# Kernel optimization log

Measured on AMD Instinct MI355X. Metric: run time of the kernel, lower is better.

## Reference

```python
import jax, jax.numpy as jnp
import numpy as np

RADIUS = 5
EPS = 1e-08


def _box_blur(x, r):
    """Normalized (2r+1)x(2r+1) box filter with reflect padding, NCHW."""
    k = 2 * r + 1
    B, C, H, W = x.shape
    xp = jnp.pad(x, ((0, 0), (0, 0), (r, r), (r, r)), mode='reflect')
    y = xp.reshape(B * C, 1, H + 2 * r, W + 2 * r)
    kh = jnp.ones((1, 1, k, 1), x.dtype) / k
    kw = jnp.ones((1, 1, 1, k), x.dtype) / k
    y = jax.lax.conv_general_dilated(y, kh, (1, 1), 'VALID')
    y = jax.lax.conv_general_dilated(y, kw, (1, 1), 'VALID')
    return y.reshape(B, C, H, W)


def setup_inputs() -> dict:
    key = jax.random.key(0)
    k1, k2 = jax.random.split(key)
    feat = jax.random.uniform(k1, (8, 16, 512, 512), dtype=jnp.float32)
    img = jax.random.uniform(k2, (8, 1, 512, 512), dtype=jnp.float32)
    return {"feat": feat, "img": img}


def reference(feat, img):
    r, eps = RADIUS, EPS
    # scalar-guidance guided filter (guidance img has 1 channel)
    mean_I = _box_blur(img, r)                  # [B,1,H,W]
    mean_p = _box_blur(feat, r)                 # [B,D,H,W]
    corr_I = _box_blur(img * img, r)            # [B,1,H,W]
    corr_Ip = _box_blur(img * feat, r)          # [B,D,H,W]
    var_I = corr_I - mean_I * mean_I
    cov_Ip = corr_Ip - mean_I * mean_p
    a = cov_Ip / (var_I + eps)                  # [B,D,H,W]
    b = mean_p - a * mean_I                     # [B,D,H,W]
    mean_a = _box_blur(a, r)
    mean_b = _box_blur(b, r)
    return mean_a * img + mean_b
```

## Files before the change

### kernel.cpp

```cpp
#include <hip/hip_runtime.h>

#define HH 512
#define WW 512
#define HW (512*512)
#define NB 8
#define ND 16
#define TW 64
#define TH 64
#define VR 74
#define PT 86
#define GAP 20

__device__ __forceinline__ int reflect(int v) {
    if (v < 0) v = -v;
    if (v >= HH) v = 2*HH - 2 - v;
    return v;
}

__global__ __launch_bounds__(256) void img_stats(const float* __restrict__ img,
                                                 float2* __restrict__ miv) {
    const int VRs = 42, PTs = 86, THs = 32, TWs = 64;
    __shared__ __align__(16) float hBuf[2*VRs*PTs + 20];
    float* hF = hBuf;
    float* hP = hBuf + VRs*PTs + 20;

    int blk  = blockIdx.x;
    int tile = blk & 127;
    int b    = blk >> 7;
    int ty0  = (tile >> 3) * THs;
    int tx0  = (tile & 7)  * TWs;

    const float inv121 = 1.0f/121.0f;
    const float* ib = img + (size_t)b*HW;
    const int t = threadIdx.x;

    if (t < 252) {
        int seg = t / 84, col = t - seg*84;
        int gx = reflect(tx0 - 10 + col);
        const float* icol = ib + gx;
        int vr0 = seg*14;
        float rv[11], rq[11];
        float sv = 0.f, sq = 0.f;
        #pragma unroll
        for (int j = 0; j < 10; ++j) {
            int gy = reflect(ty0 - 10 + vr0 + j);
            float v = icol[gy*WW], q = v*v;
            rv[j] = v; rq[j] = q; sv += v; sq += q;
        }
        #pragma unroll
        for (int k = 0; k < 14; ++k) {
            int vr = vr0 + k;
            int gy = reflect(ty0 + vr);
            float v = icol[gy*WW], q = v*v;
            sv += v; sq += q;
            hF[vr*PTs + col] = sv;
            hP[vr*PTs + col] = sq;
            sv -= rv[k%11]; sq -= rq[k%11];
            rv[(k+10)%11] = v; rq[(k+10)%11] = q;
        }
    }
    __syncthreads();

    if (t < 168) {
        int arr = t & 1;
        int j2  = t >> 1;
        int seg = (j2 >= 42) ? 1 : 0;
        int vr  = j2 - seg*42;
        int xb = seg ? 38 : 0;
        int nout = seg ? 18 : 19;
        float* rA = (arr ? hP : hF) + vr*PTs;
        float2 ring[5];
        float T = 0.f;
        #pragma unroll
        for (int j = 0; j < 5; ++j) {
            float2 v = *(float2*)(rA + xb + 2*j);
            ring[j] = v; T += v.x + v.y;
        }
        #pragma unroll
        for (int k2 = 0; k2 < 19; ++k2) {
            if (k2 < nout) {
                int hc = xb + 2*k2;
                float2 p = *(float2*)(rA + hc + 10);
                float2 q = ring[k2 % 5];
                float O0 = T + p.x;
                float O1 = O0 + p.y - q.x;
                T = O1 - q.y;
                ring[k2 % 5] = p;
                float2 o; o.x = O0*inv121; o.y = O1*inv121;
                *(float2*)(rA + hc + 10*seg) = o;
            }
        }
    }
    __syncthreads();

    float2* mb = miv + (size_t)b*HW;
    for (int i = t; i < THs*TWs; i += 256) {
        int y = i >> 6, x = i & 63;
        int vr = y + 5, hc = x + 5;
        int slot = hc + ((hc >= 38) ? 10 : 0);
        float mI  = hF[vr*PTs + slot];
        float mII = hP[vr*PTs + slot];
        float var = mII - mI*mI;
        float2 o; o.x = mI; o.y = 1.0f / (var + 1e-8f);
        mb[(ty0 + y)*WW + tx0 + x] = o;
    }
}

__global__ __launch_bounds__(512) void guided_main(const float* __restrict__ feat,
                                                   const float* __restrict__ img,
                                                   const float2* __restrict__ miv,
                                                   float* __restrict__ out) {
    __shared__ __align__(16) float hBuf[2*VR*PT + GAP];
    float* hF = hBuf;
    float* hP = hBuf + VR*PT + GAP;

    int blk  = blockIdx.x;
    int tile = blk & 63;
    int bd   = blk >> 6;
    int b    = bd >> 4;
    int ty0  = (tile >> 3) * TH;
    int tx0  = (tile & 7)  * TW;

    const float inv121 = 1.0f/121.0f;
    const float* fb   = feat + (size_t)bd*HW;
    const float* ib   = img  + (size_t)b*HW;
    const float2* mivb = miv + (size_t)b*HW;
    const int t = threadIdx.x;

    if (t < 504) {
        int seg = t / 84, col = t - seg*84;
        int gx = reflect(tx0 - 10 + col);
        const float* fcol = fb + gx;
        const float* icol = ib + gx;
        int vr0 = seg*13;
        float rf[11], rp[11];
        float sf = 0.f, sp = 0.f;
        #pragma unroll
        for (int j = 0; j < 10; ++j) {
            int gy = reflect(ty0 - 10 + vr0 + j);
            float f = fcol[gy*WW], im = icol[gy*WW];
            float p = f*im;
            rf[j] = f; rp[j] = p; sf += f; sp += p;
        }
        #pragma unroll
        for (int k = 0; k < 13; ++k) {
            int vr = vr0 + k;
            if (vr < VR) {
                int gy = reflect(ty0 + vr);
                float f = fcol[gy*WW], im = icol[gy*WW];
                float p = f*im;
                sf += f; sp += p;
                hF[vr*PT + col] = sf;
                hP[vr*PT + col] = sp;
                sf -= rf[k%11]; sp -= rp[k%11];
                rf[(k+10)%11] = f; rp[(k+10)%11] = p;
            }
        }
    }
    __syncthreads();

    if (t < 296) {
        int arr = t & 1;
        int j2  = t >> 1;
        int seg = (j2 >= 74) ? 1 : 0;
        int vr  = j2 - seg*74;
        int xb = seg ? 38 : 0;
        int nout = seg ? 18 : 19;
        float* rA = (arr ? hP : hF) + vr*PT;
        float2 ring[5];
        float T = 0.f;
        #pragma unroll
        for (int j = 0; j < 5; ++j) {
            float2 v = *(float2*)(rA + xb + 2*j);
            ring[j] = v; T += v.x + v.y;
        }
        #pragma unroll
        for (int k2 = 0; k2 < 19; ++k2) {
            if (k2 < nout) {
                int hc = xb + 2*k2;
                float2 p = *(float2*)(rA + hc + 10);
                float2 q = ring[k2 % 5];
                float O0 = T + p.x;
                float O1 = O0 + p.y - q.x;
                T = O1 - q.y;
                ring[k2 % 5] = p;
                float2 o; o.x = O0*inv121; o.y = O1*inv121;
                *(float2*)(rA + hc + 10*seg) = o;
            }
        }
    }
    __syncthreads();

    for (int i = t; i < VR*37; i += 512) {
        int y = i / 37, c2 = i - y*37;
        int x0 = 2*c2;
        int slot = x0 + ((x0 >= 38) ? 10 : 0);
        float* pF = &hF[y*PT + slot];
        float* pP = &hP[y*PT + slot];
        float2 mp2  = *(float2*)pF;
        float2 cip2 = *(float2*)pP;
        int gy = reflect(ty0 - 5 + y);
        const float2* mrow = mivb + gy*WW;
        int gx0 = tx0 - 5 + x0;
        float2 g0 = mrow[reflect(gx0)];
        float2 g1 = mrow[reflect(gx0+1)];
        float a0 = (cip2.x - g0.x*mp2.x) * g0.y;
        float b0 = mp2.x - a0*g0.x;
        float a1 = (cip2.y - g1.x*mp2.y) * g1.y;
        float b1 = mp2.y - a1*g1.x;
        float2 oa; oa.x = a0; oa.y = a1;
        float2 ob2; ob2.x = b0; ob2.y = b1;
        *(float2*)pF = oa;
        *(float2*)pP = ob2;
    }
    __syncthreads();

    if (t < 148) {
        int arr = t & 1;
        int j2  = t >> 1;
        int seg = (j2 >= 37) ? 1 : 0;
        int c2  = j2 - seg*37;
        int x0 = 2*c2;
        int slotc = x0 + ((x0 >= 38) ? 10 : 0);
        int y0 = seg*32;
        float* A = (arr ? hP : hF);
        float2 ring[11];
        float sx = 0.f, sy = 0.f;
        #pragma unroll
        for (int j = 0; j < 10; ++j) {
            float2 v = *(float2*)(A + (y0+j)*PT + slotc);
            ring[j] = v; sx += v.x; sy += v.y;
        }
        #pragma unroll
        for (int k = 0; k < 32; ++k) {
            int y = y0 + k;
            float2 v = *(float2*)(A + (y+10)*PT + slotc);
            sx += v.x; sy += v.y;
            int wrow = y + 10*seg;
            float2 o; o.x = sx; o.y = sy;
            *(float2*)(A + wrow*PT + slotc) = o;
            sx -= ring[k%11].x; sy -= ring[k%11].y;
            ring[(k+10)%11] = v;
        }
    }
    __syncthreads();

    if (t < 256) {
        int arr = t & 1;
        int r2  = t >> 1;
        int seg = r2 >> 6, row = r2 & 63;
        int prow = row + ((row >= 32) ? 10 : 0);
        float* rA = (arr ? hP : hF) + prow*PT;
        int xb = seg*32;
        float2 ring[5];
        float T = 0.f;
        #pragma unroll
        for (int j = 0; j < 5; ++j) {
            int idx = xb + 2*j;
            int sl = idx + ((idx >= 38) ? 10 : 0);
            float2 v = *(float2*)(rA + sl);
            ring[j] = v; T += v.x + v.y;
        }
        #pragma unroll
        for (int k2 = 0; k2 < 16; ++k2) {
            int x = xb + 2*k2;
            int idx = x + 10;
            int sl = idx + ((idx >= 38) ? 10 : 0);
            float2 p = *(float2*)(rA + sl);
            float2 q = ring[k2 % 5];
            float O0 = T + p.x;
            float O1 = O0 + p.y - q.x;
            T = O1 - q.y;
            ring[k2 % 5] = p;
            int wcol = x + 20*seg;
            float2 o; o.x = O0; o.y = O1;
            *(float2*)(rA + wcol) = o;
        }
    }
    __syncthreads();

    float* ob = out + (size_t)bd*HW;
    for (int i = t; i < TH*32; i += 512) {
        int y = i >> 5, c2 = i & 31;
        int x0 = 2*c2;
        int prow = y + ((y >= 32) ? 10 : 0);
        int wcol = (x0 < 32) ? x0 : x0 + 20;
        float2 ma2 = *(float2*)(&hF[prow*PT + wcol]);
        float2 mb2 = *(float2*)(&hP[prow*PT + wcol]);
        int gy = ty0 + y;
        float2 im2 = *(const float2*)(ib + gy*WW + tx0 + x0);
        float2 o;
        o.x = (ma2.x*im2.x + mb2.x)*inv121;
        o.y = (ma2.y*im2.y + mb2.y)*inv121;
        *(float2*)(ob + gy*WW + tx0 + x0) = o;
    }
}

extern "C" void kernel_launch(void* const* d_in, const int* in_sizes, int n_in,
                              void* d_out, int out_size, void* d_ws, size_t ws_size,
                              hipStream_t stream) {
    const float* feat = (const float*)d_in[0];
    const float* img  = (const float*)d_in[1];
    float* out  = (float*)d_out;
    float2* miv = (float2*)d_ws;

    img_stats<<<NB*128, 256, 0, stream>>>(img, miv);
    guided_main<<<NB*ND*64, 512, 0, stream>>>(feat, img, miv, out);
}
```

Baseline: 149.3 us.

## Interleave F/P planes in shared memory as float2 pairs for wider LDS access

Replaces the two separate shared-memory planes (box sums of feat and feat*img) with a single interleaved buffer in which each column holds an (F,P) pair. The horizontal passes now process both arrays in one thread using float4 loads and stores, which halves the threads used in those phases. The a/b computation and the final output read a single float4 instead of two float2 loads. This cuts LDS instruction count but changes the bank-access patterns, and the horizontal passes now run with half as many active threads.

```diff
diff --git a/kernel.cpp b/kernel.cpp
--- a/kernel.cpp
+++ b/kernel.cpp
@@ -8,8 +8,7 @@
 #define TW 64
 #define TH 64
 #define VR 74
-#define PT 86
-#define GAP 20
+#define PTW 172
 
 __device__ __forceinline__ int reflect(int v) {
     if (v < 0) v = -v;
@@ -110,9 +109,7 @@
                                                    const float* __restrict__ img,
                                                    const float2* __restrict__ miv,
                                                    float* __restrict__ out) {
-    __shared__ __align__(16) float hBuf[2*VR*PT + GAP];
-    float* hF = hBuf;
-    float* hP = hBuf + VR*PT + GAP;
+    __shared__ __align__(16) float S[VR*PTW];
 
     int blk  = blockIdx.x;
     int tile = blk & 63;
@@ -150,8 +147,8 @@
                 float f = fcol[gy*WW], im = icol[gy*WW];
                 float p = f*im;
                 sf += f; sp += p;
-                hF[vr*PT + col] = sf;
-                hP[vr*PT + col] = sp;
+                float2 st; st.x = sf; st.y = sp;
+                *(float2*)(S + vr*PTW + 2*col) = st;
                 sf -= rf[k%11]; sp -= rp[k%11];
                 rf[(k+10)%11] = f; rp[(k+10)%11] = p;
             }
@@ -159,139 +156,128 @@
     }
     __syncthreads();
 
-    if (t < 296) {
-        int arr = t & 1;
-        int j2  = t >> 1;
-        int seg = (j2 >= 74) ? 1 : 0;
-        int vr  = j2 - seg*74;
-        int xb = seg ? 38 : 0;
+    if (t < 148) {
+        int seg = (t >= 74) ? 1 : 0;
+        int vr  = t - seg*74;
+        float* row = S + vr*PTW;
+        int xbu = seg*19;
         int nout = seg ? 18 : 19;
-        float* rA = (arr ? hP : hF) + vr*PT;
-        float2 ring[5];
-        float T = 0.f;
+        float4 ring[5];
+        float TF = 0.f, TP = 0.f;
         #pragma unroll
         for (int j = 0; j < 5; ++j) {
-            float2 v = *(float2*)(rA + xb + 2*j);
-            ring[j] = v; T += v.x + v.y;
-        }
-        #pragma unroll
-        for (int k2 = 0; k2 < 19; ++k2) {
-            if (k2 < nout) {
-                int hc = xb + 2*k2;
-                float2 p = *(float2*)(rA + hc + 10);
-                float2 q = ring[k2 % 5];
-                float O0 = T + p.x;
-                float O1 = O0 + p.y - q.x;
-                T = O1 - q.y;
-                ring[k2 % 5] = p;
-                float2 o; o.x = O0*inv121; o.y = O1*inv121;
-                *(float2*)(rA + hc + 10*seg) = o;
+            float4 v = *(float4*)(row + 4*(xbu + j));
+            ring[j] = v; TF += v.x + v.z; TP += v.y + v.w;
+        }
+        #pragma unroll
+        for (int k = 0; k < 19; ++k) {
+            if (k < nout) {
+                float4 p = *(float4*)(row + 4*(xbu + 5 + k));
+                float4 q = ring[k % 5];
+                float O0f = TF + p.x;
+                float O1f = O0f + p.z - q.x;
+                TF = O1f - q.z;
+                float O0p = TP + p.y;
+                float O1p = O0p + p.w - q.y;
+                TP = O1p - q.w;
+                ring[k % 5] = p;
+                float4 o;
+                o.x = O0f*inv121; o.y = O0p*inv121;
+                o.z = O1f*inv121; o.w = O1p*inv121;
+                *(float4*)(row + 4*(k + xbu + 5*seg)) = o;
             }
         }
     }
     __syncthreads();
 
     for (int i = t; i < VR*37; i += 512) {
-        int y = i / 37, c2 = i - y*37;
-        int x0 = 2*c2;
-        int slot = x0 + ((x0 >= 38) ? 10 : 0);
-        float* pF = &hF[y*PT + slot];
-        float* pP = &hP[y*PT + slot];
-        float2 mp2  = *(float2*)pF;
-        float2 cip2 = *(float2*)pP;
+        int y = i / 37, u = i - y*37;
+        int su = u + ((u >= 19) ? 5 : 0);
+        float* cell = S + y*PTW + 4*su;
+        float4 mc = *(float4*)cell;
         int gy = reflect(ty0 - 5 + y);
         const float2* mrow = mivb + gy*WW;
-        int gx0 = tx0 - 5 + x0;
+        int gx0 = tx0 - 5 + 2*u;
         float2 g0 = mrow[reflect(gx0)];
         float2 g1 = mrow[reflect(gx0+1)];
-        float a0 = (cip2.x - g0.x*mp2.x) * g0.y;
-        float b0 = mp2.x - a0*g0.x;
-        float a1 = (cip2.y - g1.x*mp2.y) * g1.y;
-        float b1 = mp2.y - a1*g1.x;
-        float2 oa; oa.x = a0; oa.y = a1;
-        float2 ob2; ob2.x = b0; ob2.y = b1;
-        *(float2*)pF = oa;
-        *(float2*)pP = ob2;
+        float a0 = (mc.y - g0.x*mc.x) * g0.y;
+        float b0 = mc.x - a0*g0.x;
+        float a1 = (mc.w - g1.x*mc.z) * g1.y;
+        float b1 = mc.z - a1*g1.x;
+        float4 o; o.x = a0; o.y = b0; o.z = a1; o.w = b1;
+        *(float4*)cell = o;
     }
     __syncthreads();
 
     if (t < 148) {
-        int arr = t & 1;
-        int j2  = t >> 1;
-        int seg = (j2 >= 37) ? 1 : 0;
-        int c2  = j2 - seg*37;
-        int x0 = 2*c2;
-        int slotc = x0 + ((x0 >= 38) ? 10 : 0);
-        int y0 = seg*32;
-        float* A = (arr ? hP : hF);
+        int seg = (t >= 74) ? 1 : 0;
+        int c   = t - seg*74;
+        int sw  = 2*(c + ((c >= 38) ? 10 : 0));
+        int y0  = seg*32;
         float2 ring[11];
-        float sx = 0.f, sy = 0.f;
+        float sa = 0.f, sb = 0.f;
         #pragma unroll
         for (int j = 0; j < 10; ++j) {
-            float2 v = *(float2*)(A + (y0+j)*PT + slotc);
-            ring[j] = v; sx += v.x; sy += v.y;
+            float2 v = *(float2*)(S + (y0+j)*PTW + sw);
+            ring[j] = v; sa += v.x; sb += v.y;
         }
         #pragma unroll
         for (int k = 0; k < 32; ++k) {
             int y = y0 + k;
-            float2 v = *(float2*)(A + (y+10)*PT + slotc);
-            sx += v.x; sy += v.y;
+            float2 v = *(float2*)(S + (y+10)*PTW + sw);
+            sa += v.x; sb += v.y;
             int wrow = y + 10*seg;
-            float2 o; o.x = sx; o.y = sy;
-            *(float2*)(A + wrow*PT + slotc) = o;
-            sx -= ring[k%11].x; sy -= ring[k%11].y;
+            float2 o; o.x = sa; o.y = sb;
+            *(float2*)(S + wrow*PTW + sw) = o;
+            sa -= ring[k%11].x; sb -= ring[k%11].y;
             ring[(k+10)%11] = v;
         }
     }
     __syncthreads();
 
-    if (t < 256) {
-        int arr = t & 1;
-        int r2  = t >> 1;
-        int seg = r2 >> 6, row = r2 & 63;
+    if (t < 128) {
+        int seg = t >> 6, row = t & 63;
         int prow = row + ((row >= 32) ? 10 : 0);
-        float* rA = (arr ? hP : hF) + prow*PT;
-        int xb = seg*32;
-        float2 ring[5];
-        float T = 0.f;
+        float* rw = S + prow*PTW;
+        int ub = seg*16;
+        float4 ring[5];
+        float TA = 0.f, TB = 0.f;
         #pragma unroll
         for (int j = 0; j < 5; ++j) {
-            int idx = xb + 2*j;
-            int sl = idx + ((idx >= 38) ? 10 : 0);
-            float2 v = *(float2*)(rA + sl);
-            ring[j] = v; T += v.x + v.y;
-        }
-        #pragma unroll
-        for (int k2 = 0; k2 < 16; ++k2) {
-            int x = xb + 2*k2;
-            int idx = x + 10;
-            int sl = idx + ((idx >= 38) ? 10 : 0);
-            float2 p = *(float2*)(rA + sl);
-            float2 q = ring[k2 % 5];
-            float O0 = T + p.x;
-            float O1 = O0 + p.y - q.x;
-            T = O1 - q.y;
-            ring[k2 % 5] = p;
-            int wcol = x + 20*seg;
-            float2 o; o.x = O0; o.y = O1;
-            *(float2*)(rA + wcol) = o;
+            int u = ub + j; int su = u + ((u >= 19) ? 5 : 0);
+            float4 v = *(float4*)(rw + 4*su);
+            ring[j] = v; TA += v.x + v.z; TB += v.y + v.w;
+        }
+        #pragma unroll
+        for (int k = 0; k < 16; ++k) {
+            int u = ub + 5 + k; int su = u + ((u >= 19) ? 5 : 0);
+            float4 p = *(float4*)(rw + 4*su);
+            float4 q = ring[k % 5];
+            float A0 = TA + p.x;
+            float A1 = A0 + p.z - q.x;
+            TA = A1 - q.z;
+            float B0 = TB + p.y;
+            float B1 = B0 + p.w - q.y;
+            TB = B1 - q.w;
+            ring[k % 5] = p;
+            float4 o; o.x = A0; o.y = B0; o.z = A1; o.w = B1;
+            *(float4*)(rw + 4*(ub + k) + 40*seg) = o;
         }
     }
     __syncthreads();
 
     float* ob = out + (size_t)bd*HW;
     for (int i = t; i < TH*32; i += 512) {
-        int y = i >> 5, c2 = i & 31;
-        int x0 = 2*c2;
-        int prow = y + ((y >= 32) ? 10 : 0);
-        int wcol = (x0 < 32) ? x0 : x0 + 20;
-        float2 ma2 = *(float2*)(&hF[prow*PT + wcol]);
-        float2 mb2 = *(float2*)(&hP[prow*PT + wcol]);
-        int gy = ty0 + y;
+        int row = i >> 5, u = i & 31;
+        int prow = row + ((row >= 32) ? 10 : 0);
+        int ww = 4*u + ((u >= 16) ? 40 : 0);
+        float4 s4 = *(float4*)(S + prow*PTW + ww);
+        int gy = ty0 + row;
+        int x0 = 2*u;
         float2 im2 = *(const float2*)(ib + gy*WW + tx0 + x0);
         float2 o;
-        o.x = (ma2.x*im2.x + mb2.x)*inv121;
-        o.y = (ma2.y*im2.y + mb2.y)*inv121;
+        o.x = (s4.x*im2.x + s4.y)*inv121;
+        o.y = (s4.z*im2.y + s4.w)*inv121;
         *(float2*)(ob + gy*WW + tx0 + x0) = o;
     }
 }
```

Result: slower. 153.1 us (+2.6%).
